# Kernel tuning notes

Measured on AMD Instinct MI355X. Metric: run time of the kernel, lower is better.

## Reference

```python
import jax, jax.numpy as jnp
import numpy as np

N_NODES = 100000
N_EDGES = 1600000
IN_F, HID_F, OUT_F = 128, 128, 128


def setup_inputs() -> dict:
    key = jax.random.key(0)
    ks = jax.random.split(key, 12)
    x = jax.random.normal(ks[0], (N_NODES, IN_F), dtype=jnp.float32)
    src = jax.random.randint(ks[1], (N_EDGES,), 0, N_NODES)
    dst = jax.random.randint(ks[2], (N_EDGES,), 0, N_NODES)
    s = 1.0 / np.sqrt(IN_F)
    W1_self = jax.random.uniform(ks[3], (HID_F, IN_F), minval=-s, maxval=s)
    W1_neigh = jax.random.uniform(ks[4], (HID_F, IN_F), minval=-s, maxval=s)
    b1 = jnp.zeros((HID_F,), jnp.float32)
    s2 = 1.0 / np.sqrt(HID_F)
    W2_self = jax.random.uniform(ks[5], (OUT_F, HID_F), minval=-s2, maxval=s2)
    W2_neigh = jax.random.uniform(ks[6], (OUT_F, HID_F), minval=-s2, maxval=s2)
    b2 = jnp.zeros((OUT_F,), jnp.float32)
    s3 = 1.0 / np.sqrt(OUT_F)
    W3 = jax.random.uniform(ks[7], (OUT_F, OUT_F), minval=-s3, maxval=s3)
    b3 = jax.random.uniform(ks[8], (OUT_F,), minval=-s3, maxval=s3)
    return {"x": x, "src": src, "dst": dst,
            "W1_self": W1_self, "W1_neigh": W1_neigh, "b1": b1,
            "W2_self": W2_self, "W2_neigh": W2_neigh, "b2": b2,
            "W3": W3, "b3": b3}


def _sage_conv(h, src, dst, W_self, W_neigh, b):
    # DGL SAGEConv 'mean': h_neigh = mean over in-neighbors (src -> dst)
    msg = h[src]  # [E, d] irregular gather
    summed = jax.ops.segment_sum(msg, dst, num_segments=N_NODES)  # [N, d]
    deg = jax.ops.segment_sum(jnp.ones((src.shape[0],), h.dtype), dst,
                              num_segments=N_NODES)
    h_neigh = summed / jnp.clip(deg, 1.0)[:, None]
    return h @ W_self.T + h_neigh @ W_neigh.T + b


def reference(x, src, dst, W1_self, W1_neigh, b1, W2_self, W2_neigh, b2, W3, b3):
    h = _sage_conv(x, src, dst, W1_self, W1_neigh, b1)
    h = jax.nn.relu(h)
    h = _sage_conv(h, src, dst, W2_self, W2_neigh, b2)
    return h @ W3.T + b3
```

## Files before the change

kernel.cpp:

```cpp
#include <hip/hip_runtime.h>

#define N_NODES 100000
#define N_EDGES 1600000
#define F 128
#define NSUB 32
#define SUB_NODES (N_NODES / NSUB)
#define BCAP 128
#define PCAP 65536
#define NCHUNK 8
#define NCVT ((N_NODES * F / 8 + 255) / 256)
#define BUCKET_BLOCKS 1024
#define PREP_BLOCKS (NCVT + 257)

typedef short short8 __attribute__((ext_vector_type(8)));
typedef float f32x4 __attribute__((ext_vector_type(4)));
typedef unsigned short ushort_t;
typedef ushort_t ushort8 __attribute__((ext_vector_type(8)));

__device__ __forceinline__ ushort_t f2b(float f) {
    union { float f; unsigned u; } v; v.f = f;
    unsigned r = v.u + 0x7fff + ((v.u >> 16) & 1);
    return (ushort_t)(r >> 16);
}


__global__ __launch_bounds__(256) void k_bucket_prep(
        const int* __restrict__ src, const int* __restrict__ dst,
        int2* __restrict__ pairs, int* __restrict__ gcur,
        const float* __restrict__ x, ushort_t* __restrict__ xb,
        const float* __restrict__ W1s, const float* __restrict__ W1n,
        const float* __restrict__ W2s, const float* __restrict__ W2n,
        const float* __restrict__ W3, const float* __restrict__ b2,
        const float* __restrict__ b3,
        ushort_t* __restrict__ wb, float* __restrict__ bc) {
    const int tid = threadIdx.x;

    if (blockIdx.x >= BUCKET_BLOCKS) {
        const int blk = blockIdx.x - BUCKET_BLOCKS;
        if (blk < NCVT) {
            int i = blk * 256 + tid;
            if (i >= N_NODES * F / 8) return;
            const float4* p = reinterpret_cast<const float4*>(x) + (size_t)i * 2;
            float4 a = p[0], b = p[1];
            ushort8 r;
            r[0] = f2b(a.x); r[1] = f2b(a.y); r[2] = f2b(a.z); r[3] = f2b(a.w);
            r[4] = f2b(b.x); r[5] = f2b(b.y); r[6] = f2b(b.z); r[7] = f2b(b.w);
            *reinterpret_cast<ushort8*>(xb + (size_t)i * 8) = r;
            return;
        }
        const int b = blk - NCVT;
        if (b < 128) {
            int g = b * 256 + tid;
            float v = (g < F * F) ? W1s[g] : W1n[g - F * F];
            wb[g] = f2b(v);
        } else if (b < 256) {
            int g = (b - 128) * 256 + tid;
            int m = g >> 14, rem = g & 16383, i = rem >> 7, j = rem & 127;
            const float* __restrict__ W2 = m ? W2n : W2s;
            float s = 0.f;
#pragma unroll 8
            for (int k = 0; k < F; ++k) s += W3[i * F + k] * W2[k * F + j];
            wb[2 * F * F + g] = f2b(s);
        } else if (tid < F) {
            float s = b3[tid];
#pragma unroll 8
            for (int k = 0; k < F; ++k) s += W3[tid * F + k] * b2[k];
            bc[tid] = s;
        }
        return;
    }

    __shared__ int2 lbuf[NSUB * BCAP];
    __shared__ int lcnt[NSUB], fbase[NSUB], fcnt[NSUB];
    __shared__ int sbase[NSUB + 1];
    const int lane = tid & 63, w = tid >> 6;
    if (tid < NSUB) lcnt[tid] = 0;
    __syncthreads();

    for (int base = blockIdx.x * 1024; base < N_EDGES; base += BUCKET_BLOCKS * 1024) {
#pragma unroll
        for (int r = 0; r < 4; ++r) {
            int idx = base + r * 256 + tid;
            if (idx < N_EDGES) {
                int d = dst[idx], s = src[idx];
                int p = d / SUB_NODES;
                int dl = d - p * SUB_NODES;
                int slot = atomicAdd(&lcnt[p], 1);
                if (slot < BCAP) lbuf[p * BCAP + slot] = make_int2(dl, s);
                else {
                    int g = atomicAdd(&gcur[p], 1);
                    pairs[(size_t)p * PCAP + g] = make_int2(dl, s);
                }
            }
        }
        __syncthreads();
        if (tid < NSUB) {
            int c = lcnt[tid]; if (c > BCAP) c = BCAP;
            fcnt[tid] = c;
            fbase[tid] = atomicAdd(&gcur[tid], c);
        }
        __syncthreads();
        if (w == 0) {
            int c = (lane < NSUB) ? fcnt[lane] : 0;
            int xx = c;
#pragma unroll
            for (int off = 1; off < 32; off <<= 1) {
                int y = __shfl_up(xx, off, 64);
                if (lane >= off) xx += y;
            }
            if (lane < NSUB) sbase[lane + 1] = xx;
            if (lane == 0) sbase[0] = 0;
        }
        __syncthreads();
        const int total = sbase[NSUB];
        for (int f = tid; f < total; f += 256) {
            int lo2 = 0, hi2 = NSUB;
            while (hi2 - lo2 > 1) {
                int mid = (lo2 + hi2) >> 1;
                if (sbase[mid] <= f) lo2 = mid; else hi2 = mid;
            }
            int i = f - sbase[lo2];
            pairs[(size_t)lo2 * PCAP + fbase[lo2] + i] = lbuf[lo2 * BCAP + i];
        }
        __syncthreads();
        if (tid < NSUB) lcnt[tid] = 0;
        __syncthreads();
    }
}

__global__ __launch_bounds__(1024) void k_histc(const int2* __restrict__ pairs,
                                                const int* __restrict__ gcur,
                                                int* __restrict__ hists) {
    __shared__ int hc[SUB_NODES];
    const int p = blockIdx.x / NCHUNK;
    const int c = blockIdx.x % NCHUNK;
    for (int i = threadIdx.x; i < SUB_NODES; i += 1024) hc[i] = 0;
    __syncthreads();
    const int n = gcur[p];
    const int chunk = (n + NCHUNK - 1) / NCHUNK;
    const int lo = c * chunk;
    int hi = lo + chunk; if (hi > n) hi = n;
    const int2* __restrict__ sl = pairs + (size_t)p * PCAP;
    for (int i = lo + threadIdx.x; i < hi; i += 1024) atomicAdd(&hc[sl[i].x], 1);
    __syncthreads();
    int* __restrict__ hout = hists + ((size_t)p * NCHUNK + c) * SUB_NODES;
    for (int i = threadIdx.x; i < SUB_NODES; i += 1024) hout[i] = hc[i];
}

__global__ __launch_bounds__(1024) void k_place3(const int2* __restrict__ pairs,
                                                 const int* __restrict__ gcur,
                                                 const int* __restrict__ hists,
                                                 int* __restrict__ row_ptr,
                                                 int* __restrict__ col) {
    __shared__ int cur[SUB_NODES];
    __shared__ int ws[16];
    const int t = threadIdx.x, lane = t & 63, w = t >> 6;
    const int p = blockIdx.x / NCHUNK;
    const int c = blockIdx.x % NCHUNK;
    const int* __restrict__ hp = hists + (size_t)p * NCHUNK * SUB_NODES;

    int pv = (lane < p) ? gcur[lane] : 0;
#pragma unroll
    for (int off = 32; off > 0; off >>= 1) pv += __shfl_xor(pv, off, 64);
    const int pbase = pv;

    int cnt[4], par[4];
#pragma unroll
    for (int j = 0; j < 4; ++j) {
        int i = t * 4 + j;
        int full = 0, part = 0;
        if (i < SUB_NODES) {
#pragma unroll
            for (int cc = 0; cc < NCHUNK; ++cc) {
                int hv = hp[cc * SUB_NODES + i];
                full += hv;
                if (cc < c) part += hv;
            }
        }
        cnt[j] = full; par[j] = part;
    }
    int lsum = cnt[0] + cnt[1] + cnt[2] + cnt[3];

    int x = lsum;
#pragma unroll
    for (int off = 1; off < 64; off <<= 1) {
        int y = __shfl_up(x, off, 64);
        if (lane >= off) x += y;
    }
    if (lane == 63) ws[w] = x;
    __syncthreads();
    if (w == 0) {
        int s = (lane < 16) ? ws[lane] : 0;
#pragma unroll
        for (int off = 1; off < 16; off <<= 1) {
            int y = __shfl_up(s, off, 64);
            if (lane >= off) s += y;
        }
        if (lane < 16) ws[lane] = s;
    }
    __syncthreads();
    int run = pbase + ((w == 0) ? 0 : ws[w - 1]) + x - lsum;

#pragma unroll
    for (int j = 0; j < 4; ++j) {
        int i = t * 4 + j;
        if (i < SUB_NODES) {
            cur[i] = run + par[j];
            if (c == 0) row_ptr[p * SUB_NODES + i] = run;
            run += cnt[j];
        }
    }
    if (p == 0 && c == 0 && t == 0) row_ptr[N_NODES] = N_EDGES;
    __syncthreads();

    const int n = gcur[p];
    const int chunk = (n + NCHUNK - 1) / NCHUNK;
    const int lo = c * chunk;
    int hi = lo + chunk; if (hi > n) hi = n;
    const int2* __restrict__ sl = pairs + (size_t)p * PCAP;
    for (int i = lo + t; i < hi; i += 1024) {
        int2 pr = sl[i];
        int pos = atomicAdd(&cur[pr.x], 1);
        col[pos] = pr.y;
    }
}


__global__ __launch_bounds__(256) void k_agg(const ushort_t* __restrict__ h,
                                             const int* __restrict__ row_ptr,
                                             const int* __restrict__ col,
                                             ushort_t* __restrict__ out) {
    int node = (blockIdx.x * blockDim.x + threadIdx.x) >> 6;
    if (node >= N_NODES) return;
    const int lane = threadIdx.x & 63;
    const unsigned loff = (unsigned)lane * 4u;
    const char* __restrict__ hb = reinterpret_cast<const char*>(h);
    const int beg = row_ptr[node], end = row_ptr[node + 1];
    float ax = 0.f, ay = 0.f;
    for (int e = beg; e < end; e += 8) {
        unsigned v[8];
#pragma unroll
        for (int u = 0; u < 8; ++u) {
            int idx = e + u; idx = (idx < end) ? idx : end - 1;
            unsigned s = (unsigned)col[idx];
            v[u] = *reinterpret_cast<const unsigned*>(hb + (size_t)((s << 8) + loff));
        }
#pragma unroll
        for (int u = 0; u < 8; ++u) {
            unsigned vv = (e + u < end) ? v[u] : 0u;
            ax += __uint_as_float(vv << 16);
            ay += __uint_as_float(vv & 0xffff0000u);
        }
    }
    int deg = end - beg;
    float inv = 1.0f / (float)(deg > 0 ? deg : 1);
    unsigned r = ((unsigned)f2b(ax * inv)) | (((unsigned)f2b(ay * inv)) << 16);
    *reinterpret_cast<unsigned*>(out + ((size_t)node << 7) + lane * 2) = r;
}


template <bool RELU, bool F32OUT>
__global__ __launch_bounds__(512) void k_layer(
        const ushort_t* __restrict__ A0, const ushort_t* __restrict__ A1,
        const ushort_t* __restrict__ W0, const ushort_t* __restrict__ W1,
        const float* __restrict__ bias, void* __restrict__ outv) {
    const int t = threadIdx.x;
    const int lane = t & 63;
    const int wid = t >> 6;
    const int wr = wid >> 2;
    const int wc = wid & 3;
    const int node0 = blockIdx.x * 128;
    const int arow = lane & 15;
    const int kgrp = lane >> 4;

    f32x4 acc[4][2];
#pragma unroll
    for (int fr = 0; fr < 4; ++fr)
#pragma unroll
        for (int fc = 0; fc < 2; ++fc) acc[fr][fc] = (f32x4)(0.f);

#pragma unroll
    for (int ph = 0; ph < 2; ++ph) {
        const ushort_t* __restrict__ A = ph ? A1 : A0;
        const ushort_t* __restrict__ W = ph ? W1 : W0;

        short8 bfrag[4][2];
#pragma unroll
        for (int ks = 0; ks < 4; ++ks)
#pragma unroll
            for (int fc = 0; fc < 2; ++fc) {
                int c = wc * 32 + fc * 16 + arow;
                bfrag[ks][fc] = *reinterpret_cast<const short8*>(W + c * F + ks * 32 + kgrp * 8);
            }

#pragma unroll
        for (int ks = 0; ks < 4; ++ks) {
            short8 afrag[4];
#pragma unroll
            for (int fr = 0; fr < 4; ++fr) {
                int r = node0 + wr * 64 + fr * 16 + arow;
                if (r > N_NODES - 1) r = N_NODES - 1;
                afrag[fr] = *reinterpret_cast<const short8*>(A + (size_t)r * F + ks * 32 + kgrp * 8);
            }
#pragma unroll
            for (int fr = 0; fr < 4; ++fr)
#pragma unroll
                for (int fc = 0; fc < 2; ++fc)
                    acc[fr][fc] = __builtin_amdgcn_mfma_f32_16x16x32_bf16(
                        afrag[fr], bfrag[ks][fc], acc[fr][fc], 0, 0, 0);
        }
    }

#pragma unroll
    for (int fr = 0; fr < 4; ++fr)
#pragma unroll
        for (int fc = 0; fc < 2; ++fc) {
            int c = wc * 32 + fc * 16 + (lane & 15);
            float bv = bias[c];
#pragma unroll
            for (int r4 = 0; r4 < 4; ++r4) {
                int row = node0 + wr * 64 + fr * 16 + (lane >> 4) * 4 + r4;
                if (row >= N_NODES) continue;
                float v = acc[fr][fc][r4] + bv;
                if (RELU) v = fmaxf(v, 0.f);
                if (F32OUT)
                    reinterpret_cast<float*>(outv)[(size_t)row * F + c] = v;
                else
                    reinterpret_cast<ushort_t*>(outv)[(size_t)row * F + c] = f2b(v);
            }
        }
}


extern "C" void kernel_launch(void* const* d_in, const int* in_sizes, int n_in,
                              void* d_out, int out_size, void* d_ws, size_t ws_size,
                              hipStream_t stream) {
    const float* x   = (const float*)d_in[0];
    const int*   src = (const int*)d_in[1];
    const int*   dst = (const int*)d_in[2];
    const float* W1s = (const float*)d_in[3];
    const float* W1n = (const float*)d_in[4];
    const float* b1  = (const float*)d_in[5];
    const float* W2s = (const float*)d_in[6];
    const float* W2n = (const float*)d_in[7];
    const float* b2  = (const float*)d_in[8];
    const float* W3  = (const float*)d_in[9];
    const float* b3  = (const float*)d_in[10];
    float* out = (float*)d_out;

    char* p = (char*)d_ws;
    auto align512 = [](size_t v) { return (v + 511) & ~(size_t)511; };
    int* row_ptr = (int*)p;        p += align512((N_NODES + 1) * sizeof(int));
    int* gcur    = (int*)p;        p += align512(NSUB * sizeof(int));
    int* col     = (int*)p;        p += align512((size_t)N_EDGES * sizeof(int));
    ushort_t* wb = (ushort_t*)p;   p += align512((size_t)4 * F * F * sizeof(ushort_t));
    float* bc    = (float*)p;      p += align512(F * sizeof(float));
    ushort_t* xb = (ushort_t*)p;   p += align512((size_t)N_NODES * F * sizeof(ushort_t));
    ushort_t* aggb = (ushort_t*)p; p += align512((size_t)N_NODES * F * sizeof(ushort_t));
    ushort_t* h1b  = (ushort_t*)p; p += align512((size_t)N_NODES * F * sizeof(ushort_t));
    int2* pairs = (int2*)aggb;
    int* hists = (int*)h1b;

    hipMemsetAsync(gcur, 0, NSUB * sizeof(int), stream);
    k_bucket_prep<<<BUCKET_BLOCKS + PREP_BLOCKS, 256, 0, stream>>>(
        src, dst, pairs, gcur, x, xb, W1s, W1n, W2s, W2n, W3, b2, b3, wb, bc);
    k_histc<<<NSUB * NCHUNK, 1024, 0, stream>>>(pairs, gcur, hists);
    k_place3<<<NSUB * NCHUNK, 1024, 0, stream>>>(pairs, gcur, hists, row_ptr, col);

    const int agg_grid = (N_NODES + 3) / 4;
    const int gemm_grid = (N_NODES + 127) / 128;

    k_agg<<<agg_grid, 256, 0, stream>>>(xb, row_ptr, col, aggb);
    k_layer<true, false><<<gemm_grid, 512, 0, stream>>>(
        xb, aggb, wb + 0 * F * F, wb + 1 * F * F, b1, h1b);

    k_agg<<<agg_grid, 256, 0, stream>>>(h1b, row_ptr, col, aggb);
    k_layer<false, true><<<gemm_grid, 512, 0, stream>>>(
        h1b, aggb, wb + 2 * F * F, wb + 3 * F * F, bc, out);
}
```

Before: 293.9 us.

## Fuse neighbor mean aggregation into the SAGE layer GEMM via shared memory

Each layer's block now does the neighbor gather-mean for its 128 nodes itself, one wavefront per 16 rows, and writes the bf16 means into a padded shared-memory tile. The neighbor-side MFMA then reads its A fragments from that tile instead of from a global aggregation buffer. This removes the separate aggregation kernel and the global write and read of the aggregated features. In exchange the grid is much coarser (about 782 blocks of 512 threads with a 34 KB LDS tile), which may hide the latency of the irregular gathers less well. Load imbalance inside a block also stalls its GEMM until the slowest wave finishes, and the pairs buffer gets its own workspace region.

Result: slower. 324.7 us (+10.5%).

```diff
diff --git a/kernel.cpp b/kernel.cpp
--- a/kernel.cpp
+++ b/kernel.cpp
@@ -226,50 +226,52 @@
 }
 
 
-__global__ __launch_bounds__(256) void k_agg(const ushort_t* __restrict__ h,
-                                             const int* __restrict__ row_ptr,
-                                             const int* __restrict__ col,
-                                             ushort_t* __restrict__ out) {
-    int node = (blockIdx.x * blockDim.x + threadIdx.x) >> 6;
-    if (node >= N_NODES) return;
-    const int lane = threadIdx.x & 63;
-    const unsigned loff = (unsigned)lane * 4u;
-    const char* __restrict__ hb = reinterpret_cast<const char*>(h);
-    const int beg = row_ptr[node], end = row_ptr[node + 1];
-    float ax = 0.f, ay = 0.f;
-    for (int e = beg; e < end; e += 8) {
-        unsigned v[8];
-#pragma unroll
-        for (int u = 0; u < 8; ++u) {
-            int idx = e + u; idx = (idx < end) ? idx : end - 1;
-            unsigned s = (unsigned)col[idx];
-            v[u] = *reinterpret_cast<const unsigned*>(hb + (size_t)((s << 8) + loff));
-        }
-#pragma unroll
-        for (int u = 0; u < 8; ++u) {
-            unsigned vv = (e + u < end) ? v[u] : 0u;
-            ax += __uint_as_float(vv << 16);
-            ay += __uint_as_float(vv & 0xffff0000u);
-        }
-    }
-    int deg = end - beg;
-    float inv = 1.0f / (float)(deg > 0 ? deg : 1);
-    unsigned r = ((unsigned)f2b(ax * inv)) | (((unsigned)f2b(ay * inv)) << 16);
-    *reinterpret_cast<unsigned*>(out + ((size_t)node << 7) + lane * 2) = r;
-}
-
-
 template <bool RELU, bool F32OUT>
-__global__ __launch_bounds__(512) void k_layer(
-        const ushort_t* __restrict__ A0, const ushort_t* __restrict__ A1,
+__global__ __launch_bounds__(512) void k_agg_layer(
+        const ushort_t* __restrict__ A,
+        const int* __restrict__ row_ptr, const int* __restrict__ col,
         const ushort_t* __restrict__ W0, const ushort_t* __restrict__ W1,
         const float* __restrict__ bias, void* __restrict__ outv) {
+    __shared__ ushort_t sN[128][136];
     const int t = threadIdx.x;
     const int lane = t & 63;
     const int wid = t >> 6;
+    const int node0 = blockIdx.x * 128;
+    const char* __restrict__ hb = reinterpret_cast<const char*>(A);
+    const unsigned loff = (unsigned)lane * 4u;
+
+    for (int i = 0; i < 16; ++i) {
+        const int row = wid * 16 + i;
+        const int node = node0 + row;
+        float ax = 0.f, ay = 0.f;
+        if (node < N_NODES) {
+            const int beg = row_ptr[node], end = row_ptr[node + 1];
+            for (int e = beg; e < end; e += 8) {
+                unsigned v[8];
+#pragma unroll
+                for (int u = 0; u < 8; ++u) {
+                    int idx = e + u; idx = (idx < end) ? idx : end - 1;
+                    unsigned s = (unsigned)col[idx];
+                    v[u] = *reinterpret_cast<const unsigned*>(hb + (size_t)((s << 8) + loff));
+                }
+#pragma unroll
+                for (int u = 0; u < 8; ++u) {
+                    unsigned vv = (e + u < end) ? v[u] : 0u;
+                    ax += __uint_as_float(vv << 16);
+                    ay += __uint_as_float(vv & 0xffff0000u);
+                }
+            }
+            int deg = end - beg;
+            float inv = 1.0f / (float)(deg > 0 ? deg : 1);
+            ax *= inv; ay *= inv;
+        }
+        unsigned r = ((unsigned)f2b(ax)) | (((unsigned)f2b(ay)) << 16);
+        *reinterpret_cast<unsigned*>(&sN[row][lane * 2]) = r;
+    }
+    __syncthreads();
+
     const int wr = wid >> 2;
     const int wc = wid & 3;
-    const int node0 = blockIdx.x * 128;
     const int arow = lane & 15;
     const int kgrp = lane >> 4;
 
@@ -279,20 +281,15 @@
 #pragma unroll
         for (int fc = 0; fc < 2; ++fc) acc[fr][fc] = (f32x4)(0.f);
 
-#pragma unroll
-    for (int ph = 0; ph < 2; ++ph) {
-        const ushort_t* __restrict__ A = ph ? A1 : A0;
-        const ushort_t* __restrict__ W = ph ? W1 : W0;
-
+    {
         short8 bfrag[4][2];
 #pragma unroll
         for (int ks = 0; ks < 4; ++ks)
 #pragma unroll
             for (int fc = 0; fc < 2; ++fc) {
                 int c = wc * 32 + fc * 16 + arow;
-                bfrag[ks][fc] = *reinterpret_cast<const short8*>(W + c * F + ks * 32 + kgrp * 8);
-            }
-
+                bfrag[ks][fc] = *reinterpret_cast<const short8*>(W0 + c * F + ks * 32 + kgrp * 8);
+            }
 #pragma unroll
         for (int ks = 0; ks < 4; ++ks) {
             short8 afrag[4];
@@ -301,6 +298,31 @@
                 int r = node0 + wr * 64 + fr * 16 + arow;
                 if (r > N_NODES - 1) r = N_NODES - 1;
                 afrag[fr] = *reinterpret_cast<const short8*>(A + (size_t)r * F + ks * 32 + kgrp * 8);
+            }
+#pragma unroll
+            for (int fr = 0; fr < 4; ++fr)
+#pragma unroll
+                for (int fc = 0; fc < 2; ++fc)
+                    acc[fr][fc] = __builtin_amdgcn_mfma_f32_16x16x32_bf16(
+                        afrag[fr], bfrag[ks][fc], acc[fr][fc], 0, 0, 0);
+        }
+    }
+    {
+        short8 bfrag[4][2];
+#pragma unroll
+        for (int ks = 0; ks < 4; ++ks)
+#pragma unroll
+            for (int fc = 0; fc < 2; ++fc) {
+                int c = wc * 32 + fc * 16 + arow;
+                bfrag[ks][fc] = *reinterpret_cast<const short8*>(W1 + c * F + ks * 32 + kgrp * 8);
+            }
+#pragma unroll
+        for (int ks = 0; ks < 4; ++ks) {
+            short8 afrag[4];
+#pragma unroll
+            for (int fr = 0; fr < 4; ++fr) {
+                int r = wr * 64 + fr * 16 + arow;
+                afrag[fr] = *reinterpret_cast<const short8*>(&sN[r][ks * 32 + kgrp * 8]);
             }
 #pragma unroll
             for (int fr = 0; fr < 4; ++fr)
@@ -356,9 +378,8 @@
     ushort_t* wb = (ushort_t*)p;   p += align512((size_t)4 * F * F * sizeof(ushort_t));
     float* bc    = (float*)p;      p += align512(F * sizeof(float));
     ushort_t* xb = (ushort_t*)p;   p += align512((size_t)N_NODES * F * sizeof(ushort_t));
-    ushort_t* aggb = (ushort_t*)p; p += align512((size_t)N_NODES * F * sizeof(ushort_t));
-    ushort_t* h1b  = (ushort_t*)p; p += align512((size_t)N_NODES * F * sizeof(ushort_t));
-    int2* pairs = (int2*)aggb;
+    int2* pairs  = (int2*)p;       p += align512((size_t)NSUB * PCAP * sizeof(int2));
+    ushort_t* h1b = (ushort_t*)p;  p += align512((size_t)N_NODES * F * sizeof(ushort_t));
     int* hists = (int*)h1b;
 
     hipMemsetAsync(gcur, 0, NSUB * sizeof(int), stream);
@@ -367,14 +388,11 @@
     k_histc<<<NSUB * NCHUNK, 1024, 0, stream>>>(pairs, gcur, hists);
     k_place3<<<NSUB * NCHUNK, 1024, 0, stream>>>(pairs, gcur, hists, row_ptr, col);
 
-    const int agg_grid = (N_NODES + 3) / 4;
     const int gemm_grid = (N_NODES + 127) / 128;
 
-    k_agg<<<agg_grid, 256, 0, stream>>>(xb, row_ptr, col, aggb);
-    k_layer<true, false><<<gemm_grid, 512, 0, stream>>>(
-        xb, aggb, wb + 0 * F * F, wb + 1 * F * F, b1, h1b);
-
-    k_agg<<<agg_grid, 256, 0, stream>>>(h1b, row_ptr, col, aggb);
-    k_layer<false, true><<<gemm_grid, 512, 0, stream>>>(
-        h1b, aggb, wb + 2 * F * F, wb + 3 * F * F, bc, out);
-}
+    k_agg_layer<true, false><<<gemm_grid, 512, 0, stream>>>(
+        xb, row_ptr, col, wb + 0 * F * F, wb + 1 * F * F, b1, h1b);
+
+    k_agg_layer<false, true><<<gemm_grid, 512, 0, stream>>>(
+        h1b, row_ptr, col, wb + 2 * F * F, wb + 3 * F * F, bc, out);
+}
```
